# Kernel tuning notes

Hardware: AMD Instinct MI355X
Metric: run time of the kernel (lower is better)

## Reference

```python
import jax, jax.numpy as jnp
import numpy as np

B, S, E, H = 4, 2048, 1024, 16
DK = E // H  # 64


def setup_inputs() -> dict:
    key = jax.random.key(0)
    ks = jax.random.split(key, 6)
    scale = 1.0 / np.sqrt(E)
    return {
        "x": jax.random.normal(ks[0], (B, S, E), dtype=jnp.float32),
        "Wq": jax.random.normal(ks[1], (E, E), dtype=jnp.float32) * scale,
        "Wk": jax.random.normal(ks[2], (E, E), dtype=jnp.float32) * scale,
        "Wv": jax.random.normal(ks[3], (E, E), dtype=jnp.float32) * scale,
        "Wo": jax.random.normal(ks[4], (E, E), dtype=jnp.float32) * scale,
        "theta": jax.random.normal(ks[5], (DK,), dtype=jnp.float32),
    }


def _heads(t):
    # [B,S,E] -> [B,H,S,DK]
    b, s, _ = t.shape
    return t.reshape(b, s, H, DK).transpose(0, 2, 1, 3)


def reference(x, Wq, Wk, Wv, Wo, theta):
    # nn.Linear (no bias): y = x @ W.T
    # quantum transform: independent single-qubit RX(x)->RX(theta)->  <Z> = cos(x+theta)
    q = jnp.cos(_heads(x @ Wq.T) + theta)  # [B,H,S,DK]
    k = jnp.cos(_heads(x @ Wk.T) + theta)
    v = jnp.cos(_heads(x @ Wv.T) + theta)
    scores = jnp.einsum("bhqd,bhkd->bhqk", q, k) / jnp.sqrt(jnp.float32(DK))
    attn = jax.nn.softmax(scores, axis=-1)  # dropout is identity in eval
    out = jnp.einsum("bhqk,bhkd->bhqd", attn, v)  # [B,H,S,DK]
    out = out.transpose(0, 2, 1, 3).reshape(x.shape[0], -1, E)
    return out @ Wo.T
```

## Files before the change

kernel.cpp:

```cpp
#include <hip/hip_runtime.h>

#define B_  4
#define S_  2048
#define E_  1024
#define H_  16
#define DK_ 64
#define M_  (B_*S_)

typedef __attribute__((ext_vector_type(8)))  short short8;
typedef __attribute__((ext_vector_type(4)))  float f32x4;
typedef __attribute__((ext_vector_type(16))) float f32x16;

#define QSCALE 0.18033688f

__device__ __forceinline__ unsigned short f2b(float f) {
    union { float f; unsigned u; } v; v.f = f;
    unsigned u = v.u;
    return (unsigned short)((u + 0x7fffu + ((u >> 16) & 1u)) >> 16);
}

__device__ __forceinline__ void gload_lds16(const unsigned short* g, unsigned short* l) {
    __builtin_amdgcn_global_load_lds((const __attribute__((address_space(1))) void*)g,
                                     (__attribute__((address_space(3))) void*)l, 16, 0, 0);
}

#define XN4 (M_*E_/4)
#define WN4 (E_*E_/4)
__global__ __launch_bounds__(256) void cvt_all(
    const float* __restrict__ x,
    const float* __restrict__ w0, const float* __restrict__ w1,
    const float* __restrict__ w2, const float* __restrict__ w3,
    unsigned short* __restrict__ xb, unsigned short* __restrict__ wb,
    unsigned short* __restrict__ wob) {
    int i = blockIdx.x * 256 + threadIdx.x;
    const float* src;
    unsigned short* dst;
    int idx;
    if (i < XN4) { src = x; dst = xb; idx = i; }
    else {
        int j = i - XN4;
        int z = j >> 18;
        idx = j & (WN4 - 1);
        src = (z == 0) ? w0 : (z == 1) ? w1 : (z == 2) ? w2 : w3;
        dst = (z < 3) ? wb + (size_t)z * E_ * E_ : wob;
    }
    float4 f = ((const float4*)src)[idx];
    ushort4 o;
    o.x = f2b(f.x); o.y = f2b(f.y); o.z = f2b(f.z); o.w = f2b(f.w);
    ((ushort4*)dst)[idx] = o;
}

__global__ __launch_bounds__(256) void gemm_qkv(
    const unsigned short* __restrict__ xb,
    const unsigned short* __restrict__ Wb,
    const float* __restrict__ theta,
    unsigned short* __restrict__ qb,
    unsigned short* __restrict__ kb,
    unsigned short* __restrict__ vtb)
{
    __shared__ unsigned short smem[128*144];
    unsigned short* As = smem;
    unsigned short* Bs = smem + 128*64;
    const int tid = threadIdx.x;
    const int w = tid >> 6, lane = tid & 63, quad = lane >> 4, col = lane & 15;
    const int wm = (w & 1) * 64, wn = (w >> 1) * 64;
    const int m0 = blockIdx.x * 128, n0 = blockIdx.y * 128, z = blockIdx.z;
    const unsigned short* Wz = Wb + (size_t)z * E_ * E_;
    const int srow = lane >> 3, schunk = (lane & 7) * 8;

    f32x4 acc[4][4] = {};
    for (int k0 = 0; k0 < E_; k0 += 64) {
        #pragma unroll
        for (int c = 0; c < 4; c++) {
            int row = w*32 + c*8 + srow;
            gload_lds16(&xb[(size_t)(m0+row)*E_ + k0 + schunk], &As[(w*32 + c*8)*64]);
            gload_lds16(&Wz[(size_t)(n0+row)*E_ + k0 + schunk], &Bs[(w*32 + c*8)*64]);
        }
        __syncthreads();
        #pragma unroll
        for (int kk = 0; kk < 64; kk += 32) {
            short8 a[4], b[4];
            #pragma unroll
            for (int i = 0; i < 4; i++)
                a[i] = *(const short8*)&As[(wm + i*16 + col)*64 + kk + quad*8];
            #pragma unroll
            for (int j = 0; j < 4; j++)
                b[j] = *(const short8*)&Bs[(wn + j*16 + col)*64 + kk + quad*8];
            #pragma unroll
            for (int i = 0; i < 4; i++)
                #pragma unroll
                for (int j = 0; j < 4; j++)
                    acc[i][j] = __builtin_amdgcn_mfma_f32_16x16x32_bf16(a[i], b[j], acc[i][j], 0, 0, 0);
        }
        __syncthreads();
    }

    const int bblk = m0 >> 11;
    const int sbase = m0 & (S_-1);

    if (z != 2) {
        const float qs = (z == 0) ? QSCALE : 1.0f;
        #pragma unroll
        for (int j = 0; j < 4; j++) {
            int nl = wn + j*16 + col;
            float th = theta[(n0 + nl) & 63];
            #pragma unroll
            for (int i = 0; i < 4; i++)
                #pragma unroll
                for (int r = 0; r < 4; r++) {
                    int ml = wm + i*16 + quad*4 + r;
                    int nls = nl ^ (((ml >> 2) & 3) << 4);
                    smem[ml*144 + nls] = f2b(__cosf(acc[i][j][r] + th) * qs);
                }
        }
        __syncthreads();
        unsigned short* dst = (z == 0) ? qb : kb;
        const int h0 = n0 >> 6;
        #pragma unroll
        for (int k = 0; k < 8; k++) {
            int idx = k*256 + tid;
            int chunk = idx & 7, seg = idx >> 3;
            int ml = seg >> 1, hh = seg & 1;
            int ch = chunk ^ (((ml >> 2) & 3) << 1);
            int4 val = *(const int4*)&smem[ml*144 + hh*64 + ch*8];
            size_t g = ((size_t)(bblk*H_ + h0 + hh)*S_ + sbase + ml)*DK_ + chunk*8;
            *(int4*)&dst[g] = val;
        }
    } else {
        #pragma unroll
        for (int j = 0; j < 4; j++) {
            int nl = wn + j*16 + col;
            float th = theta[(n0 + nl) & 63];
            #pragma unroll
            for (int i = 0; i < 4; i++)
                #pragma unroll
                for (int r = 0; r < 4; r++)
                    smem[nl*136 + wm + i*16 + quad*4 + r] = f2b(__cosf(acc[i][j][r] + th));
        }
        __syncthreads();
        int row = tid >> 1, halfm = (tid & 1) * 64;
        int n = n0 + row, h = n >> 6, d = n & 63;
        size_t base = ((size_t)(bblk*H_ + h)*DK_ + d)*S_ + sbase + halfm;
        #pragma unroll
        for (int k = 0; k < 8; k++)
            *(int4*)&vtb[base + k*8] = *(const int4*)&smem[row*136 + halfm + k*8];
    }
}

__global__ __launch_bounds__(256) void gemm_out(
    const unsigned short* __restrict__ ctx,
    const unsigned short* __restrict__ Wob,
    float* __restrict__ out)
{
    __shared__ unsigned short As[128*64];
    __shared__ unsigned short Bs[128*64];
    const int tid = threadIdx.x;
    const int w = tid >> 6, lane = tid & 63, quad = lane >> 4, col = lane & 15;
    const int wm = (w & 1) * 64, wn = (w >> 1) * 64;
    const int m0 = blockIdx.x * 128, n0 = blockIdx.y * 128;
    const int srow = lane >> 3, schunk = (lane & 7) * 8;

    f32x4 acc[4][4] = {};
    for (int k0 = 0; k0 < E_; k0 += 64) {
        #pragma unroll
        for (int c = 0; c < 4; c++) {
            int row = w*32 + c*8 + srow;
            gload_lds16(&ctx[(size_t)(m0+row)*E_ + k0 + schunk], &As[(w*32 + c*8)*64]);
            gload_lds16(&Wob[(size_t)(n0+row)*E_ + k0 + schunk], &Bs[(w*32 + c*8)*64]);
        }
        __syncthreads();
        #pragma unroll
        for (int kk = 0; kk < 64; kk += 32) {
            short8 a[4], b[4];
            #pragma unroll
            for (int i = 0; i < 4; i++)
                a[i] = *(const short8*)&As[(wm + i*16 + col)*64 + kk + quad*8];
            #pragma unroll
            for (int j = 0; j < 4; j++)
                b[j] = *(const short8*)&Bs[(wn + j*16 + col)*64 + kk + quad*8];
            #pragma unroll
            for (int i = 0; i < 4; i++)
                #pragma unroll
                for (int j = 0; j < 4; j++)
                    acc[i][j] = __builtin_amdgcn_mfma_f32_16x16x32_bf16(a[i], b[j], acc[i][j], 0, 0, 0);
        }
        __syncthreads();
    }
    #pragma unroll
    for (int j = 0; j < 4; j++) {
        int n = n0 + wn + j*16 + col;
        #pragma unroll
        for (int i = 0; i < 4; i++)
            #pragma unroll
            for (int r = 0; r < 4; r++) {
                int m = m0 + wm + i*16 + quad*4 + r;
                out[(size_t)m*E_ + n] = acc[i][j][r];
            }
    }
}

#define LPK 72

__global__ __launch_bounds__(256, 4) void flash_attn(
    const unsigned short* __restrict__ qb,
    const unsigned short* __restrict__ kb,
    const unsigned short* __restrict__ vtb,
    unsigned short* __restrict__ ctx)
{
    __shared__ unsigned short Kt[64*LPK];
    __shared__ unsigned short Vt[64*LPK];
    const int tid = threadIdx.x;
    const int w = tid >> 6, lane = tid & 63, col = lane & 31, half = lane >> 5;
    const int q0 = blockIdx.x * 128;
    const int bh = blockIdx.y;

    short8 qf[4];
    {
        const unsigned short* qrow = qb + ((size_t)bh*S_ + q0 + w*32 + col)*DK_;
        #pragma unroll
        for (int c = 0; c < 4; c++)
            qf[c] = *(const short8*)&qrow[c*16 + half*8];
    }

    union U8 { unsigned u[4]; short8 s8; };
    U8 ones;
    #pragma unroll
    for (int i = 0; i < 4; i++) ones.u[i] = 0x3F803F80u;

    f32x16 oacc[2] = {};
    f32x16 lacc = {};

    for (int kt = 0; kt < S_; kt += 64) {
        __syncthreads();
        for (int i = tid; i < 512; i += 256) {
            int row = i >> 3, c8 = (i & 7) * 8;
            *(int4*)&Kt[row*LPK + c8] = *(const int4*)&kb [((size_t)bh*S_  + kt + row)*DK_ + c8];
            *(int4*)&Vt[row*LPK + c8] = *(const int4*)&vtb[((size_t)bh*DK_ + row)*S_ + kt + c8];
        }
        __syncthreads();

        #pragma unroll
        for (int t = 0; t < 2; t++) {
            f32x16 sacc = {};
            #pragma unroll
            for (int c = 0; c < 4; c++) {
                short8 kf = *(const short8*)&Kt[(t*32 + col)*LPK + c*16 + half*8];
                sacc = __builtin_amdgcn_mfma_f32_32x32x16_bf16(kf, qf[c], sacc, 0, 0, 0);
            }
            unsigned pk[4][2], pp[4][2];
            #pragma unroll
            for (int rg = 0; rg < 4; rg++) {
                float p0 = __builtin_amdgcn_exp2f(sacc[rg*4+0]);
                float p1 = __builtin_amdgcn_exp2f(sacc[rg*4+1]);
                float p2 = __builtin_amdgcn_exp2f(sacc[rg*4+2]);
                float p3 = __builtin_amdgcn_exp2f(sacc[rg*4+3]);
                pk[rg][0] = __builtin_amdgcn_perm(__float_as_uint(p1), __float_as_uint(p0), 0x07060302u);
                pk[rg][1] = __builtin_amdgcn_perm(__float_as_uint(p3), __float_as_uint(p2), 0x07060302u);
            }
            #pragma unroll
            for (int rg = 0; rg < 4; rg++) {
                pp[rg][0] = __shfl_xor((int)pk[rg][0], 32);
                pp[rg][1] = __shfl_xor((int)pk[rg][1], 32);
            }
            #pragma unroll
            for (int kc = 0; kc < 2; kc++) {
                const int lo = 2*kc, hi = 2*kc + 1;
                U8 pa;
                pa.u[0] = half ? pp[hi][0] : pk[lo][0];
                pa.u[1] = half ? pp[hi][1] : pk[lo][1];
                pa.u[2] = half ? pk[hi][0] : pp[lo][0];
                pa.u[3] = half ? pk[hi][1] : pp[lo][1];
                lacc = __builtin_amdgcn_mfma_f32_32x32x16_bf16(pa.s8, ones.s8, lacc, 0, 0, 0);
                #pragma unroll
                for (int dt = 0; dt < 2; dt++) {
                    short8 vf = *(const short8*)&Vt[(dt*32 + col)*LPK + t*32 + kc*16 + half*8];
                    oacc[dt] = __builtin_amdgcn_mfma_f32_32x32x16_bf16(pa.s8, vf, oacc[dt], 0, 0, 0);
                }
            }
        }
    }

    const int b = bh >> 4, h = bh & 15;
    #pragma unroll
    for (int rg = 0; rg < 4; rg++)
        #pragma unroll
        for (int rr = 0; rr < 4; rr++) {
            int row = rr + rg*8 + half*4;
            float inv = 1.0f / lacc[rg*4 + rr];
            int s = q0 + w*32 + row;
            size_t rowoff = ((size_t)(b*S_ + s))*E_ + h*64;
            #pragma unroll
            for (int dt = 0; dt < 2; dt++)
                ctx[rowoff + dt*32 + col] = f2b(oacc[dt][rg*4 + rr] * inv);
        }
}

extern "C" void kernel_launch(void* const* d_in, const int* in_sizes, int n_in,
                              void* d_out, int out_size, void* d_ws, size_t ws_size,
                              hipStream_t stream) {
    (void)in_sizes; (void)n_in; (void)out_size; (void)ws_size;
    const float* x     = (const float*)d_in[0];
    const float* Wq    = (const float*)d_in[1];
    const float* Wk    = (const float*)d_in[2];
    const float* Wv    = (const float*)d_in[3];
    const float* Wo    = (const float*)d_in[4];
    const float* theta = (const float*)d_in[5];
    float* out = (float*)d_out;

    unsigned short* ws  = (unsigned short*)d_ws;
    unsigned short* xb  = ws;
    unsigned short* Wb  = xb  + (size_t)M_*E_;
    unsigned short* Wob = Wb  + (size_t)3*E_*E_;
    unsigned short* qb  = Wob + (size_t)E_*E_;
    unsigned short* kb  = qb  + (size_t)B_*H_*S_*DK_;
    unsigned short* vtb = kb  + (size_t)B_*H_*S_*DK_;
    unsigned short* ctx = xb;

    cvt_all<<<(XN4 + 4*WN4)/256, 256, 0, stream>>>(x, Wq, Wk, Wv, Wo, xb, Wb, Wob);

    gemm_qkv<<<dim3(M_/128, E_/128, 3), 256, 0, stream>>>(xb, Wb, theta, qb, kb, vtb);
    flash_attn<<<dim3(S_/128, B_*H_), 256, 0, stream>>>(qb, kb, vtb, ctx);
    gemm_out<<<dim3(M_/128, E_/128), 256, 0, stream>>>(ctx, Wob, out);
}
```

Baseline: 300.6 us.

## Double-buffer K/V tiles with register prefetch, permlane swap, and block swizzle

The attention kernel now double-buffers K and V tiles in LDS. The next tile is prefetched into registers while MFMAs run on the current one, and there is one barrier per iteration instead of two. The cross-half shuffle of P is replaced with permlane32_swap, s_setprio is raised around the MFMA sections, and block indices are swizzled to group blocks of the same head. The aim is to hide global load latency and cut shuffle and barrier overhead, at the cost of doubled LDS and extra registers, which may lower occupancy.

Result: faster. 290.1 us (-3.5%).

```diff
diff --git a/kernel.cpp b/kernel.cpp
--- a/kernel.cpp
+++ b/kernel.cpp
@@ -207,12 +207,20 @@
     const unsigned short* __restrict__ vtb,
     unsigned short* __restrict__ ctx)
 {
-    __shared__ unsigned short Kt[64*LPK];
-    __shared__ unsigned short Vt[64*LPK];
+    __shared__ unsigned short Kt[2][64*LPK];
+    __shared__ unsigned short Vt[2][64*LPK];
     const int tid = threadIdx.x;
     const int w = tid >> 6, lane = tid & 63, col = lane & 31, half = lane >> 5;
-    const int q0 = blockIdx.x * 128;
-    const int bh = blockIdx.y;
+
+    const int f   = blockIdx.y * gridDim.x + blockIdx.x;
+    const int swz = (f & 7) * 128 + (f >> 3);
+    const int q0  = (swz & 15) * 128;
+    const int bh  = swz >> 4;
+
+    const unsigned short* kbase = kb  + (size_t)bh * S_ * DK_;
+    const unsigned short* vbase = vtb + (size_t)bh * DK_ * S_;
+    const int srow = tid >> 3;
+    const int sc8  = (tid & 7) * 8;
 
     short8 qf[4];
     {
@@ -230,24 +238,38 @@
     f32x16 oacc[2] = {};
     f32x16 lacc = {};
 
-    for (int kt = 0; kt < S_; kt += 64) {
-        __syncthreads();
-        for (int i = tid; i < 512; i += 256) {
-            int row = i >> 3, c8 = (i & 7) * 8;
-            *(int4*)&Kt[row*LPK + c8] = *(const int4*)&kb [((size_t)bh*S_  + kt + row)*DK_ + c8];
-            *(int4*)&Vt[row*LPK + c8] = *(const int4*)&vtb[((size_t)bh*DK_ + row)*S_ + kt + c8];
-        }
-        __syncthreads();
+    #pragma unroll
+    for (int u = 0; u < 2; u++) {
+        *(int4*)&Kt[0][(srow + u*32)*LPK + sc8] =
+            *(const int4*)&kbase[(size_t)(srow + u*32)*DK_ + sc8];
+        *(int4*)&Vt[0][(srow + u*32)*LPK + sc8] =
+            *(const int4*)&vbase[(size_t)(srow + u*32)*S_ + sc8];
+    }
+    __syncthreads();
+
+    for (int it = 0; it < S_/64; ++it) {
+        const int cur = it & 1, nxt = cur ^ 1;
+        const int ktn = it*64 + 64;
+        int4 rk[2], rv[2];
+        if (ktn < S_) {
+            #pragma unroll
+            for (int u = 0; u < 2; u++) {
+                rk[u] = *(const int4*)&kbase[(size_t)(ktn + srow + u*32)*DK_ + sc8];
+                rv[u] = *(const int4*)&vbase[(size_t)(srow + u*32)*S_ + ktn + sc8];
+            }
+        }
 
         #pragma unroll
         for (int t = 0; t < 2; t++) {
             f32x16 sacc = {};
+            __builtin_amdgcn_s_setprio(1);
             #pragma unroll
             for (int c = 0; c < 4; c++) {
-                short8 kf = *(const short8*)&Kt[(t*32 + col)*LPK + c*16 + half*8];
+                short8 kf = *(const short8*)&Kt[cur][(t*32 + col)*LPK + c*16 + half*8];
                 sacc = __builtin_amdgcn_mfma_f32_32x32x16_bf16(kf, qf[c], sacc, 0, 0, 0);
             }
-            unsigned pk[4][2], pp[4][2];
+            __builtin_amdgcn_s_setprio(0);
+            unsigned pk[4][2];
             #pragma unroll
             for (int rg = 0; rg < 4; rg++) {
                 float p0 = __builtin_amdgcn_exp2f(sacc[rg*4+0]);
@@ -258,26 +280,34 @@
                 pk[rg][1] = __builtin_amdgcn_perm(__float_as_uint(p3), __float_as_uint(p2), 0x07060302u);
             }
             #pragma unroll
-            for (int rg = 0; rg < 4; rg++) {
-                pp[rg][0] = __shfl_xor((int)pk[rg][0], 32);
-                pp[rg][1] = __shfl_xor((int)pk[rg][1], 32);
-            }
-            #pragma unroll
             for (int kc = 0; kc < 2; kc++) {
                 const int lo = 2*kc, hi = 2*kc + 1;
+                auto s0 = __builtin_amdgcn_permlane32_swap((int)pk[lo][0], (int)pk[hi][0], false, false);
+                auto s1 = __builtin_amdgcn_permlane32_swap((int)pk[lo][1], (int)pk[hi][1], false, false);
                 U8 pa;
-                pa.u[0] = half ? pp[hi][0] : pk[lo][0];
-                pa.u[1] = half ? pp[hi][1] : pk[lo][1];
-                pa.u[2] = half ? pk[hi][0] : pp[lo][0];
-                pa.u[3] = half ? pk[hi][1] : pp[lo][1];
+                pa.u[0] = (unsigned)s0[0];
+                pa.u[1] = (unsigned)s1[0];
+                pa.u[2] = (unsigned)s0[1];
+                pa.u[3] = (unsigned)s1[1];
+                __builtin_amdgcn_s_setprio(1);
                 lacc = __builtin_amdgcn_mfma_f32_32x32x16_bf16(pa.s8, ones.s8, lacc, 0, 0, 0);
                 #pragma unroll
                 for (int dt = 0; dt < 2; dt++) {
-                    short8 vf = *(const short8*)&Vt[(dt*32 + col)*LPK + t*32 + kc*16 + half*8];
+                    short8 vf = *(const short8*)&Vt[cur][(dt*32 + col)*LPK + t*32 + kc*16 + half*8];
                     oacc[dt] = __builtin_amdgcn_mfma_f32_32x32x16_bf16(pa.s8, vf, oacc[dt], 0, 0, 0);
                 }
-            }
-        }
+                __builtin_amdgcn_s_setprio(0);
+            }
+        }
+
+        if (ktn < S_) {
+            #pragma unroll
+            for (int u = 0; u < 2; u++) {
+                *(int4*)&Kt[nxt][(srow + u*32)*LPK + sc8] = rk[u];
+                *(int4*)&Vt[nxt][(srow + u*32)*LPK + sc8] = rv[u];
+            }
+        }
+        __syncthreads();
     }
 
     const int b = bh >> 4, h = bh & 15;
```
